# Performance work log

Measured on AMD Instinct MI355X. Metric: run time of the kernel, lower is better.

## Reference

```python
import jax, jax.numpy as jnp
import numpy as np

S = 30.0   # scale
M = 0.3    # arcface angular margin
EPS = 1e-07


def setup_inputs() -> dict:
    key = jax.random.key(0)
    k1, k2 = jax.random.split(key)
    N, C = 4096, 32000
    x = jax.random.normal(k1, (N, C), dtype=jnp.float32)
    target = jax.random.randint(k2, (N,), 0, C, dtype=jnp.int64)
    return {"x": x, "target": target}


def reference(x, target):
    # Row-wise L2 normalize (F.normalize, dim=1)
    norm = jnp.sqrt(jnp.sum(x * x, axis=1, keepdims=True))
    xn = x / jnp.maximum(norm, 1e-12)                      # (N, C)
    # Target-column cosine per row
    cos_t = jnp.take_along_axis(xn, target[:, None], axis=1)[:, 0]  # (N,)
    # ArcFace numerator: s * cos(acos(clamp(cos_t)) + m)
    theta = jnp.arccos(jnp.clip(cos_t, -1.0 + EPS, 1.0 - EPS))
    numerator = S * jnp.cos(theta + M)
    # Denominator: exp(numerator) + sum_{j != y} exp(s * xn_j)
    # = exp(numerator) + full row sum - target term (fused masked reduction)
    row_sum = jnp.sum(jnp.exp(S * xn), axis=1)             # (N,)
    denominator = jnp.exp(numerator) + row_sum - jnp.exp(S * cos_t)
    L = numerator - jnp.log(denominator)
    return -jnp.mean(L)
```

## Files before the change

kernel.cpp:

```cpp
#include <hip/hip_runtime.h>
#include <math.h>

#define ROWS      4096
#define COLS      32000
#define COLS4     8000
#define BLK       1024
#define NWAVES    (BLK / 64)
#define K_ITERS   8

#define S_SCALE   30.0f
#define COS_M     0.95533648912560601964f
#define SIN_M     0.29552020666133957511f

__global__ void arcface_row_kernel(const float* __restrict__ x,
                                   const int* __restrict__ target,
                                   float* __restrict__ rowL) {
    const int row = blockIdx.x;
    const int tid = threadIdx.x;
    const int lane = tid & 63;
    const int wave = tid >> 6;

    const float4* __restrict__ rowp =
        reinterpret_cast<const float4*>(x + (size_t)row * COLS);

    __shared__ float red[NWAVES];
    __shared__ float s_inv;

    float4 v[K_ITERS];
    float ss = 0.0f;
    #pragma unroll
    for (int k = 0; k < K_ITERS; ++k) {
        const int idx = k * BLK + tid;
        if (idx < COLS4) {
            v[k] = rowp[idx];
            ss += v[k].x * v[k].x + v[k].y * v[k].y
                + v[k].z * v[k].z + v[k].w * v[k].w;
        }
    }

    #pragma unroll
    for (int off = 32; off > 0; off >>= 1) ss += __shfl_down(ss, off, 64);
    if (lane == 0) red[wave] = ss;
    __syncthreads();
    if (tid == 0) {
        float tot = 0.0f;
        #pragma unroll
        for (int w = 0; w < NWAVES; ++w) tot += red[w];
        const float norm = sqrtf(tot);
        s_inv = 1.0f / fmaxf(norm, 1e-12f);
    }
    __syncthreads();
    const float inv = s_inv;
    const float sinv = S_SCALE * inv;

    float es = 0.0f;
    #pragma unroll
    for (int k = 0; k < K_ITERS; ++k) {
        const int idx = k * BLK + tid;
        if (idx < COLS4) {
            es += __expf(sinv * v[k].x) + __expf(sinv * v[k].y)
                + __expf(sinv * v[k].z) + __expf(sinv * v[k].w);
        }
    }
    #pragma unroll
    for (int off = 32; off > 0; off >>= 1) es += __shfl_down(es, off, 64);
    if (lane == 0) red[wave] = es;
    __syncthreads();

    if (tid == 0) {
        float row_sum = 0.0f;
        #pragma unroll
        for (int w = 0; w < NWAVES; ++w) row_sum += red[w];

        const int   tgt   = target[row];
        const float xt    = x[(size_t)row * COLS + tgt];
        const float cos_t = xt * inv;

        const float c = fminf(fmaxf(cos_t, -1.0f + 1e-7f), 1.0f - 1e-7f);
        const float sin_t = sqrtf(fmaxf(1.0f - c * c, 0.0f));
        const float numerator = S_SCALE * (c * COS_M - sin_t * SIN_M);

        const float denom = __expf(numerator) + row_sum - __expf(S_SCALE * cos_t);
        rowL[row] = numerator - logf(denom);
    }
}

__global__ void arcface_final_kernel(const float* __restrict__ rowL,
                                     float* __restrict__ out) {
    __shared__ float red[4];
    const int tid = threadIdx.x;
    float s = 0.0f;
    for (int i = tid; i < ROWS; i += 256) s += rowL[i];
    #pragma unroll
    for (int off = 32; off > 0; off >>= 1) s += __shfl_down(s, off, 64);
    if ((tid & 63) == 0) red[tid >> 6] = s;
    __syncthreads();
    if (tid == 0) {
        const float tot = red[0] + red[1] + red[2] + red[3];
        out[0] = -(tot / (float)ROWS);
    }
}

extern "C" void kernel_launch(void* const* d_in, const int* in_sizes, int n_in,
                              void* d_out, int out_size, void* d_ws, size_t ws_size,
                              hipStream_t stream) {
    const float* x      = (const float*)d_in[0];
    const int*   target = (const int*)d_in[1];
    float*       out    = (float*)d_out;
    float*       rowL   = (float*)d_ws;

    arcface_row_kernel<<<ROWS, BLK, 0, stream>>>(x, target, rowL);
    arcface_final_kernel<<<1, 256, 0, stream>>>(rowL, out);
}
```

Baseline: 94.14 us.

## Use nontemporal loads, hoist target gather, widen final reduction

Row data is now read with nontemporal vector loads, and the target-element gather moves to the kernel start so its latency overlaps the main loads. It also adds launch bounds, swaps logf for __logf, and rewrites the final reduction to use 1024 threads with one vector load each. The aim is to cut cache pollution and tail latency in a bandwidth-bound kernel. The risks are that nontemporal hints may not help on this cache hierarchy and that __logf is slightly less accurate.

```diff
diff --git a/kernel.cpp b/kernel.cpp
--- a/kernel.cpp
+++ b/kernel.cpp
@@ -12,27 +12,36 @@
 #define COS_M     0.95533648912560601964f
 #define SIN_M     0.29552020666133957511f
 
-__global__ void arcface_row_kernel(const float* __restrict__ x,
-                                   const int* __restrict__ target,
-                                   float* __restrict__ rowL) {
+typedef float vfloat4 __attribute__((ext_vector_type(4)));
+
+__global__ __launch_bounds__(BLK)
+void arcface_row_kernel(const float* __restrict__ x,
+                        const int* __restrict__ target,
+                        float* __restrict__ rowL) {
     const int row = blockIdx.x;
     const int tid = threadIdx.x;
     const int lane = tid & 63;
     const int wave = tid >> 6;
 
-    const float4* __restrict__ rowp =
-        reinterpret_cast<const float4*>(x + (size_t)row * COLS);
+    const vfloat4* __restrict__ rowp =
+        reinterpret_cast<const vfloat4*>(x + (size_t)row * COLS);
 
     __shared__ float red[NWAVES];
     __shared__ float s_inv;
 
-    float4 v[K_ITERS];
+    float xt = 0.0f;
+    if (tid == 0) {
+        const int tgt = target[row];
+        xt = x[(size_t)row * COLS + tgt];
+    }
+
+    vfloat4 v[K_ITERS];
     float ss = 0.0f;
     #pragma unroll
     for (int k = 0; k < K_ITERS; ++k) {
         const int idx = k * BLK + tid;
         if (idx < COLS4) {
-            v[k] = rowp[idx];
+            v[k] = __builtin_nontemporal_load(&rowp[idx]);
             ss += v[k].x * v[k].x + v[k].y * v[k].y
                 + v[k].z * v[k].z + v[k].w * v[k].w;
         }
@@ -72,8 +81,6 @@
         #pragma unroll
         for (int w = 0; w < NWAVES; ++w) row_sum += red[w];
 
-        const int   tgt   = target[row];
-        const float xt    = x[(size_t)row * COLS + tgt];
         const float cos_t = xt * inv;
 
         const float c = fminf(fmaxf(cos_t, -1.0f + 1e-7f), 1.0f - 1e-7f);
@@ -81,22 +88,25 @@
         const float numerator = S_SCALE * (c * COS_M - sin_t * SIN_M);
 
         const float denom = __expf(numerator) + row_sum - __expf(S_SCALE * cos_t);
-        rowL[row] = numerator - logf(denom);
+        rowL[row] = numerator - __logf(denom);
     }
 }
 
-__global__ void arcface_final_kernel(const float* __restrict__ rowL,
-                                     float* __restrict__ out) {
-    __shared__ float red[4];
+__global__ __launch_bounds__(1024)
+void arcface_final_kernel(const float* __restrict__ rowL,
+                          float* __restrict__ out) {
+    __shared__ float red[16];
     const int tid = threadIdx.x;
-    float s = 0.0f;
-    for (int i = tid; i < ROWS; i += 256) s += rowL[i];
+    const vfloat4 v = reinterpret_cast<const vfloat4*>(rowL)[tid];
+    float s = v.x + v.y + v.z + v.w;
     #pragma unroll
     for (int off = 32; off > 0; off >>= 1) s += __shfl_down(s, off, 64);
     if ((tid & 63) == 0) red[tid >> 6] = s;
     __syncthreads();
     if (tid == 0) {
-        const float tot = red[0] + red[1] + red[2] + red[3];
+        float tot = 0.0f;
+        #pragma unroll
+        for (int w = 0; w < 16; ++w) tot += red[w];
         out[0] = -(tot / (float)ROWS);
     }
 }
@@ -110,5 +120,5 @@
     float*       rowL   = (float*)d_ws;
 
     arcface_row_kernel<<<ROWS, BLK, 0, stream>>>(x, target, rowL);
-    arcface_final_kernel<<<1, 256, 0, stream>>>(rowL, out);
+    arcface_final_kernel<<<1, 1024, 0, stream>>>(rowL, out);
 }
```

Measured after the change: 82.48 us (median of 2 runs). -12.4%, faster.
